# Kernel optimization log

Measured on AMD Instinct MI355X. Metric: run time of the kernel, lower is better.

The kernel has to match this reference:

```python
import jax, jax.numpy as jnp
import numpy as np

B, N, D = 8, 8192, 512
H, WIDTH = 8, 2048
DH = D // H
EPS = 1e-5


def _ln(x, g, b):
    m = jnp.mean(x, axis=-1, keepdims=True)
    v = jnp.mean(jnp.square(x - m), axis=-1, keepdims=True)
    return (x - m) * jax.lax.rsqrt(v + EPS) * g + b


def setup_inputs() -> dict:
    key = jax.random.key(0)
    ks = jax.random.split(key, 16)
    s = 0.02
    return {
        "x": jax.random.normal(ks[0], (B, N, D), dtype=jnp.float32),
        "mask": jnp.ones((B, N), dtype=jnp.float32),
        "Wq": jax.random.normal(ks[1], (D, D), dtype=jnp.float32) * s,
        "bq": jnp.zeros((D,), dtype=jnp.float32),
        "Wk": jax.random.normal(ks[2], (D, D), dtype=jnp.float32) * s,
        "bk": jnp.zeros((D,), dtype=jnp.float32),
        "Wv": jax.random.normal(ks[3], (D, D), dtype=jnp.float32) * s,
        "bv": jnp.zeros((D,), dtype=jnp.float32),
        "q_alpha": jax.random.normal(ks[4], (H, DH), dtype=jnp.float32),
        "k_beta": jax.random.normal(ks[5], (H, DH), dtype=jnp.float32),
        "Wo": jax.random.normal(ks[6], (D, D), dtype=jnp.float32) * s,
        "bo": jnp.zeros((D,), dtype=jnp.float32),
        "ln0_g": jnp.ones((D,), dtype=jnp.float32),
        "ln0_b": jnp.zeros((D,), dtype=jnp.float32),
        "ln1_g": jnp.ones((D,), dtype=jnp.float32),
        "ln1_b": jnp.zeros((D,), dtype=jnp.float32),
        "W1": jax.random.normal(ks[7], (WIDTH, D), dtype=jnp.float32) * s,
        "b1": jnp.zeros((WIDTH,), dtype=jnp.float32),
        "W2": jax.random.normal(ks[8], (D, WIDTH), dtype=jnp.float32) * s,
        "b2": jnp.zeros((D,), dtype=jnp.float32),
    }


def reference(x, mask, Wq, bq, Wk, bk, Wv, bv, q_alpha, k_beta, Wo, bo,
              ln0_g, ln0_b, ln1_g, ln1_b, W1, b1, W2, b2):
    scale = DH ** -0.5
    mask_ = mask[..., None]                       # [B,N,1]
    valid = (mask != 0)[..., None]                # [B,N,1] bool, broadcast over H

    residual = x
    xn = _ln(x, ln0_g, ln0_b) * mask_

    Q = (xn @ Wq.T + bq).reshape(B, N, H, DH)
    K = (xn @ Wk.T + bk).reshape(B, N, H, DH)
    V = (xn @ Wv.T + bv).reshape(B, N, H, DH)

    # stage 1: global query pooling
    alpha = jnp.einsum('bnhd,hd->bnh', Q, q_alpha) * scale
    alpha = jnp.where(valid, alpha, -jnp.inf)
    alpha = jax.nn.softmax(alpha, axis=1)         # softmax over N
    global_q = jnp.einsum('bnhd,bnh->bhd', Q, alpha)

    # stage 2: global value pooling
    P = K * global_q[:, None]                     # [B,N,H,DH]
    beta = jnp.einsum('bnhd,hd->bnh', P, k_beta) * scale
    beta = jnp.where(valid, beta, -jnp.inf)
    beta = jax.nn.softmax(beta, axis=1)
    global_v = jnp.einsum('bnhd,bnh->bhd', V, beta)

    out = (Q + global_v[:, None]).reshape(B, N, D)
    out = out @ Wo.T + bo
    x = residual + out

    residual = x
    xn = _ln(x, ln1_g, ln1_b)
    h = jax.nn.gelu(xn @ W1.T + b1, approximate=False)
    h = jax.nn.gelu(h @ W2.T + b2, approximate=False)
    x = residual + h
    x = x * mask_
    return x
```

## Files before the change

kernel.cpp:

```cpp
#include <hip/hip_runtime.h>
#include <hip/hip_bf16.h>
#include <hip/hip_fp8.h>
#include <math.h>

typedef short s8v __attribute__((ext_vector_type(8)));
typedef short s4v __attribute__((ext_vector_type(4)));
typedef __bf16 bf8v __attribute__((ext_vector_type(8)));
typedef float f4v __attribute__((ext_vector_type(4)));
typedef long l2v __attribute__((ext_vector_type(2)));

#define GLOBAL_AS __attribute__((address_space(1)))
#define LDS_AS __attribute__((address_space(3)))

static __device__ __forceinline__ float bf2f(ushort u) {
  return __builtin_bit_cast(float, (unsigned int)u << 16);
}
static __device__ __forceinline__ ushort f2bf(float f) {
  unsigned int u = __builtin_bit_cast(unsigned int, f);
  u += 0x7FFFu + ((u >> 16) & 1u);
  return (ushort)(u >> 16);
}
static __device__ __forceinline__ unsigned char f2fp8(float f) {
#if __has_builtin(__builtin_amdgcn_cvt_pk_fp8_f32)
  int p = __builtin_amdgcn_cvt_pk_fp8_f32(f, f, 0, false);
  return (unsigned char)(p & 0xFF);
#else
  __hip_fp8_e4m3 v(f);
  return (unsigned char)v.__x;
#endif
}
static __device__ __forceinline__ float gelu_f(float v) {
  float t = v * v;
  float u = v * (0.0356774081f * t + 0.7978845608f);
  float e = __expf(-2.0f * u);
  return v * __builtin_amdgcn_rcpf(1.0f + e);
}
static __device__ __forceinline__ float wave_max_f(float v) {
  #pragma unroll
  for (int o = 32; o >= 1; o >>= 1) v = fmaxf(v, __shfl_xor(v, o));
  return v;
}
static __device__ __forceinline__ float wave_sum_f(float v) {
  #pragma unroll
  for (int o = 32; o >= 1; o >>= 1) v += __shfl_xor(v, o);
  return v;
}
static __device__ __forceinline__ void gload16(const void* g, const void* l) {
  __builtin_amdgcn_global_load_lds(
      (const GLOBAL_AS unsigned int*)g,
      (LDS_AS unsigned int*)l, 16, 0, 0);
}

__global__ void cvt_f32_fp8il(const float* __restrict__ in,
                              unsigned char* __restrict__ out, int n, int kmask) {
  int i = (blockIdx.x * 256 + threadIdx.x) * 4;
  if (i >= n) return;
  float4 v = *(const float4*)(in + i);
  const int k = i & kmask;
  const int r = k & 63;
  const int qq = (r >> 3) & 3, h = (r >> 5) & 1, j = r & 7;
  const long o = (long)(i - r) + qq * 16 + h * 8 + j;
  uchar4 ob;
  ob.x = f2fp8(v.x * 8.f); ob.y = f2fp8(v.y * 8.f);
  ob.z = f2fp8(v.z * 8.f); ob.w = f2fp8(v.w * 8.f);
  *(uchar4*)(out + o) = ob;
}

__global__ void cvt_w1_fp8il(const float* __restrict__ in,
                             unsigned char* __restrict__ out) {
  int i = (blockIdx.x * 256 + threadIdx.x) * 4;
  const int ro = i >> 9;
  const int k4 = i & 511;
  const int g = ro >> 6, fr = ro & 63;
  const int L = fr & 15, nn = fr >> 4;
  const int sr = g * 64 + ((L >> 1) & 1) * 32 + (L >> 2) * 8 + (L & 1) * 4 + nn;
  float4 v = *(const float4*)(in + (long)sr * 512 + k4);
  const int r = k4 & 63;
  const int o = (k4 - r) + ((r >> 3) & 3) * 16 + (r >> 5) * 8 + (r & 7);
  uchar4 ob;
  ob.x = f2fp8(v.x * 8.f); ob.y = f2fp8(v.y * 8.f);
  ob.z = f2fp8(v.z * 8.f); ob.w = f2fp8(v.w * 8.f);
  *(uchar4*)(out + (long)ro * 512 + o) = ob;
}

__global__ void perm_b1(const float* __restrict__ b1, float* __restrict__ b1p) {
  const int p = blockIdx.x * 256 + threadIdx.x;
  const int g = p >> 6, r = p & 63;
  const int kc = ((r >> 3) & 1) * 32 + (r >> 4) * 8 + ((r >> 2) & 1) * 4 + (r & 3);
  b1p[p] = b1[g * 64 + kc];
}

__global__ __launch_bounds__(256) void transpose512(
    const float* __restrict__ in, float* __restrict__ out) {
  __shared__ float t[32][33];
  const int bx = blockIdx.x & 15, by = blockIdx.x >> 4;
  const int tx = threadIdx.x & 31, ty = threadIdx.x >> 5;
  #pragma unroll
  for (int i = 0; i < 4; ++i)
    t[ty + i * 8][tx] = in[(long)(by * 32 + ty + i * 8) * 512 + bx * 32 + tx];
  __syncthreads();
  #pragma unroll
  for (int i = 0; i < 4; ++i)
    out[(long)(bx * 32 + ty + i * 8) * 512 + by * 32 + tx] = t[tx][ty + i * 8];
}

__global__ __launch_bounds__(256) void wqo_kernel(
    const float* __restrict__ Wo, const float* __restrict__ Wq,
    ushort* __restrict__ WqoB)
{
  __shared__ float lO[64][33];
  __shared__ float lQ[32][65];
  const int t = threadIdx.x;
  const int bi = (blockIdx.x & 7) * 64, bj = (blockIdx.x >> 3) * 64;
  float acc[16] = {};
  for (int k0 = 0; k0 < 512; k0 += 32) {
    __syncthreads();
    {
      const int r = t >> 2, c = (t & 3) * 8;
      #pragma unroll
      for (int j = 0; j < 8; ++j) lO[r][c + j] = Wo[(long)(bi + r) * 512 + k0 + c + j];
      const int r2 = t >> 3, c2 = (t & 7) * 8;
      #pragma unroll
      for (int j = 0; j < 8; ++j) lQ[r2][c2 + j] = Wq[(long)(k0 + r2) * 512 + bj + c2 + j];
    }
    __syncthreads();
    const int j = t & 63, ig = t >> 6;
    for (int kk = 0; kk < 32; ++kk) {
      float q = lQ[kk][j];
      #pragma unroll
      for (int ii = 0; ii < 16; ++ii) acc[ii] += lO[ig * 16 + ii][kk] * q;
    }
  }
  const int j = t & 63, ig = t >> 6;
  #pragma unroll
  for (int ii = 0; ii < 16; ++ii)
    WqoB[(long)(bi + ig * 16 + ii) * 512 + bj + j] = f2bf(acc[ii]);
}

__global__ __launch_bounds__(256) void wa_kernel(
    const float* __restrict__ qa, const float* __restrict__ Wq,
    const float* __restrict__ bqv, ushort* __restrict__ waB, float* __restrict__ ca)
{
  __shared__ float ql[64];
  const int h = blockIdx.x;
  const int t = threadIdx.x;
  if (h >= 8) {
    waB[h * 512 + t] = 0; waB[h * 512 + 256 + t] = 0;
    if (t == 0) ca[h] = 0.f;
    return;
  }
  if (t < 64) ql[t] = qa[h * 64 + t];
  __syncthreads();
  #pragma unroll
  for (int half = 0; half < 2; ++half) {
    const int k = half * 256 + t;
    float s = 0;
    for (int dd = 0; dd < 64; ++dd) s += ql[dd] * Wq[(long)(h * 64 + dd) * 512 + k];
    waB[h * 512 + k] = f2bf(s);
  }
  if (t == 0) {
    float s = 0;
    for (int dd = 0; dd < 64; ++dd) s += ql[dd] * bqv[h * 64 + dd];
    ca[h] = s;
  }
}

__global__ __launch_bounds__(256) void ln_rows(
    const float* __restrict__ x, const float* __restrict__ gam,
    const float* __restrict__ bet, const float* __restrict__ mask,
    ushort* __restrict__ out)
{
  const int tid = threadIdx.x, lane = tid & 63, wv = tid >> 6;
  const long row = (long)blockIdx.x * 4 + wv;
  const float* xp = x + row * 512 + lane * 8;
  float4 a = *(const float4*)xp;
  float4 b = *(const float4*)(xp + 4);
  float s = a.x + a.y + a.z + a.w + b.x + b.y + b.z + b.w;
  float q = a.x*a.x + a.y*a.y + a.z*a.z + a.w*a.w
          + b.x*b.x + b.y*b.y + b.z*b.z + b.w*b.w;
  s = wave_sum_f(s); q = wave_sum_f(q);
  float m = s * (1.f / 512.f);
  float var = q * (1.f / 512.f) - m * m;
  float r = rsqrtf(var + 1e-5f);
  float mk = mask ? mask[row] : 1.f;
  const float* gp = gam + lane * 8;
  const float* bp = bet + lane * 8;
  float4 g0 = *(const float4*)gp, g1 = *(const float4*)(gp + 4);
  float4 c0 = *(const float4*)bp, c1 = *(const float4*)(bp + 4);
  s8v o;
  o[0] = (short)f2bf(((a.x - m) * r * g0.x + c0.x) * mk);
  o[1] = (short)f2bf(((a.y - m) * r * g0.y + c0.y) * mk);
  o[2] = (short)f2bf(((a.z - m) * r * g0.z + c0.z) * mk);
  o[3] = (short)f2bf(((a.w - m) * r * g0.w + c0.w) * mk);
  o[4] = (short)f2bf(((b.x - m) * r * g1.x + c1.x) * mk);
  o[5] = (short)f2bf(((b.y - m) * r * g1.y + c1.y) * mk);
  o[6] = (short)f2bf(((b.z - m) * r * g1.z + c1.z) * mk);
  o[7] = (short)f2bf(((b.w - m) * r * g1.w + c1.w) * mk);
  *(s8v*)(out + row * 512 + lane * 8) = o;
}

__global__ __launch_bounds__(256) void ln_rows_fp8il(
    const ushort* __restrict__ x, const float* __restrict__ gam,
    const float* __restrict__ bet, unsigned char* __restrict__ out)
{
  const int tid = threadIdx.x, lane = tid & 63, wv = tid >> 6;
  const long row = (long)blockIdx.x * 4 + wv;
  s8v v = *(const s8v*)(x + row * 512 + lane * 8);
  float xv[8];
  #pragma unroll
  for (int j = 0; j < 8; ++j) xv[j] = bf2f((ushort)v[j]);
  float s = 0.f, q = 0.f;
  #pragma unroll
  for (int j = 0; j < 8; ++j) { s += xv[j]; q += xv[j] * xv[j]; }
  s = wave_sum_f(s); q = wave_sum_f(q);
  float m = s * (1.f / 512.f);
  float var = q * (1.f / 512.f) - m * m;
  float r = rsqrtf(var + 1e-5f);
  const float* gp = gam + lane * 8;
  const float* bp = bet + lane * 8;
  float4 g0 = *(const float4*)gp, g1 = *(const float4*)(gp + 4);
  float4 c0 = *(const float4*)bp, c1 = *(const float4*)(bp + 4);
  float gg[8] = {g0.x, g0.y, g0.z, g0.w, g1.x, g1.y, g1.z, g1.w};
  float cc[8] = {c0.x, c0.y, c0.z, c0.w, c1.x, c1.y, c1.z, c1.w};
  unsigned long long pk = 0;
  #pragma unroll
  for (int j = 0; j < 8; ++j) {
    unsigned char b8 = f2fp8((xv[j] - m) * r * gg[j] + cc[j]);
    pk |= (unsigned long long)b8 << (8 * j);
  }
  *(unsigned long long*)(out + row * 512 + (lane >> 3) * 64
                         + (lane & 3) * 16 + ((lane >> 2) & 1) * 8) = pk;
}

template<int BS, int CS>
__global__ __launch_bounds__(256) void logits_k(
    const ushort* __restrict__ XN, const ushort* __restrict__ Wl,
    const float* __restrict__ cvec, const float* __restrict__ mask,
    float* __restrict__ outL)
{
  __shared__ ushort lw[16 * 512];
  const int tid = threadIdx.x, lane = tid & 63, wv = tid >> 6;
  const long r0 = (long)blockIdx.x * 64;
  const int b = (int)(r0 >> 13);
  #pragma unroll
  for (int i = 0; i < 4; ++i) {
    const int u = tid + i * 256;
    const int h2 = u >> 6, uu = u & 63;
    s8v v = *(const s8v*)(Wl + (long)b * BS + h2 * 512 + uu * 8);
    *(s8v*)(lw + h2 * 512 + (uu ^ (h2 & 7)) * 8) = v;
  }
  __syncthreads();
  const int h = lane & 15, q = lane >> 4;
  const long rw = r0 + wv * 16;
  const ushort* ap = XN + (rw + (lane & 15)) * 512 + q * 8;
  f4v acc = {};
  #pragma unroll
  for (int t = 0; t < 16; ++t) {
    bf8v a = *(const bf8v*)(ap + t * 32);
    bf8v bb = *(const bf8v*)(lw + h * 512 + (((t * 4 + q) ^ (h & 7))) * 8);
    acc = __builtin_amdgcn_mfma_f32_16x16x32_bf16(a, bb, acc, 0, 0, 0);
  }
  const float cv = cvec[b * CS + h];
  #pragma unroll
  for (int j = 0; j < 4; ++j) {
    const long n = rw + q * 4 + j;
    float v = (acc[j] + cv) * 0.125f;
    if (mask[n] == 0.f) v = -1e30f;
    if (h < 8) outL[((long)((b << 3) + h) << 13) + (n & 8191)] = v;
  }
}

__global__ __launch_bounds__(1024) void softmax_rows(float* __restrict__ L)
{
  __shared__ float red[16];
  __shared__ float bc;
  const int tid = threadIdx.x, lane = tid & 63, wv = tid >> 6;
  float* p = L + ((long)blockIdx.x << 13) + tid * 8;
  float4 v0 = *(float4*)p;
  float4 v1 = *(float4*)(p + 4);
  float m = fmaxf(fmaxf(fmaxf(v0.x, v0.y), fmaxf(v0.z, v0.w)),
                  fmaxf(fmaxf(v1.x, v1.y), fmaxf(v1.z, v1.w)));
  m = wave_max_f(m);
  if (lane == 0) red[wv] = m;
  __syncthreads();
  if (tid < 64) {
    float t = (lane < 16) ? red[lane] : -INFINITY;
    t = wave_max_f(t);
    if (lane == 0) bc = t;
  }
  __syncthreads();
  const float gm = bc;
  v0.x = __expf(v0.x - gm); v0.y = __expf(v0.y - gm);
  v0.z = __expf(v0.z - gm); v0.w = __expf(v0.w - gm);
  v1.x = __expf(v1.x - gm); v1.y = __expf(v1.y - gm);
  v1.z = __expf(v1.z - gm); v1.w = __expf(v1.w - gm);
  float s = v0.x + v0.y + v0.z + v0.w + v1.x + v1.y + v1.z + v1.w;
  s = wave_sum_f(s);
  __syncthreads();
  if (lane == 0) red[wv] = s;
  __syncthreads();
  if (tid < 64) {
    float t = (lane < 16) ? red[lane] : 0.f;
    t = wave_sum_f(t);
    if (lane == 0) bc = t;
  }
  __syncthreads();
  const float inv = 1.0f / bc;
  v0.x *= inv; v0.y *= inv; v0.z *= inv; v0.w *= inv;
  v1.x *= inv; v1.y *= inv; v1.z *= inv; v1.w *= inv;
  *(float4*)p = v0;
  *(float4*)(p + 4) = v1;
}

__global__ __launch_bounds__(256) void pool_w(
    const ushort* __restrict__ XN, const float* __restrict__ wbuf,
    float* __restrict__ part)
{
  __shared__ float wlds[128][8];
  __shared__ float cmb[4][512];
  const int tid = threadIdx.x;
  const int b = blockIdx.x >> 6, ch = blockIdx.x & 63;
  const long g0 = ((long)b << 13) + ch * 128;
  if (tid < 128) {
    #pragma unroll
    for (int h = 0; h < 8; ++h)
      wlds[tid][h] = wbuf[(((long)(b * 8 + h)) << 13) + ch * 128 + tid];
  }
  __syncthreads();
  const int rg = tid >> 6, c8 = (tid & 63) * 8;
  f4v acc[8][2] = {};
  for (int it = 0; it < 32; ++it) {
    const int r = it * 4 + rg;
    s8v xv = *(const s8v*)(XN + (g0 + r) * 512 + c8);
    float xf[8];
    #pragma unroll
    for (int j = 0; j < 8; ++j) xf[j] = bf2f((ushort)xv[j]);
    #pragma unroll
    for (int h = 0; h < 8; ++h) {
      const float w = wlds[r][h];
      #pragma unroll
      for (int j = 0; j < 8; ++j) acc[h][j >> 2][j & 3] += w * xf[j];
    }
  }
  #pragma unroll
  for (int h = 0; h < 8; ++h) {
    __syncthreads();
    #pragma unroll
    for (int j = 0; j < 8; ++j) cmb[rg][c8 + j] = acc[h][j >> 2][j & 3];
    __syncthreads();
    const int col = tid * 2;
    float s0 = cmb[0][col] + cmb[1][col] + cmb[2][col] + cmb[3][col];
    float s1 = cmb[0][col + 1] + cmb[1][col + 1] + cmb[2][col + 1] + cmb[3][col + 1];
    *(float2*)(part + (((long)blockIdx.x * 8 + h) << 9) + col) = make_float2(s0, s1);
  }
}

__global__ __launch_bounds__(256) void combine_px(
    const float* __restrict__ part, float* __restrict__ px)
{
  const int bh = blockIdx.x;
  const int b = bh >> 3, h = bh & 7;
  const int col = threadIdx.x * 2;
  float s0 = 0.f, s1 = 0.f;
  for (int ch = 0; ch < 64; ++ch) {
    const float* p = part + (((long)((b * 64 + ch) * 8 + h)) << 9) + col;
    s0 += p[0]; s1 += p[1];
  }
  px[(bh << 9) + col] = s0;
  px[(bh << 9) + col + 1] = s1;
}

__global__ __launch_bounds__(64) void prep_gq_wb(
    const float* __restrict__ px, const float* __restrict__ WqT,
    const float* __restrict__ bqv, const float* __restrict__ kbv,
    const float* __restrict__ Wk, const float* __restrict__ bkv,
    ushort* __restrict__ wbB, float* __restrict__ cbs)
{
  __shared__ float pxl[512];
  __shared__ float gkb[64];
  const int bh = blockIdx.x, b = bh >> 3, h = bh & 7, d = threadIdx.x;
  #pragma unroll
  for (int i = 0; i < 8; ++i) pxl[d + i * 64] = px[(bh << 9) + d + i * 64];
  __syncthreads();
  float acc = bqv[h * 64 + d];
  for (int c = 0; c < 512; ++c) acc += pxl[c] * WqT[(long)c * 512 + h * 64 + d];
  gkb[d] = acc * kbv[h * 64 + d];
  __syncthreads();
  float s[8] = {};
  for (int dd = 0; dd < 64; ++dd) {
    const float g = gkb[dd];
    const float* wr = Wk + (long)(h * 64 + dd) * 512 + d;
    #pragma unroll
    for (int ki = 0; ki < 8; ++ki) s[ki] += g * wr[ki * 64];
  }
  #pragma unroll
  for (int ki = 0; ki < 8; ++ki)
    wbB[(long)(b * 16 + h) * 512 + d + ki * 64] = f2bf(s[ki]);
  if (d == 0) {
    float t = 0.f;
    for (int dd = 0; dd < 64; ++dd) t += gkb[dd] * bkv[h * 64 + dd];
    cbs[b * 16 + h] = t;
  }
  if (h == 0) {
    #pragma unroll
    for (int hp = 8; hp < 16; ++hp)
      for (int k = d; k < 512; k += 64) wbB[(long)(b * 16 + hp) * 512 + k] = 0;
    if (d < 8) cbs[b * 16 + 8 + d] = 0.f;
  }
}

__global__ __launch_bounds__(64) void prep_gv(
    const float* __restrict__ pv, const float* __restrict__ WvT,
    const float* __restrict__ bvv, const float* __restrict__ bqv,
    float* __restrict__ gvb)
{
  __shared__ float pxl[512];
  const int bh = blockIdx.x, b = bh >> 3, h = bh & 7, d = threadIdx.x;
  #pragma unroll
  for (int i = 0; i < 8; ++i) pxl[d + i * 64] = pv[(bh << 9) + d + i * 64];
  __syncthreads();
  float acc = bvv[h * 64 + d] + bqv[h * 64 + d];
  for (int c = 0; c < 512; ++c) acc += pxl[c] * WvT[(long)c * 512 + h * 64 + d];
  gvb[b * 512 + h * 64 + d] = acc;
}

__global__ __launch_bounds__(256) void bias_gv(
    const float* __restrict__ gv, const float* __restrict__ Wo,
    const float* __restrict__ bo, float* __restrict__ bo2) {
  const int b = blockIdx.x;
  const int n = blockIdx.y * 256 + threadIdx.x;
  const float* g = gv + b * 512;
  const float* w = Wo + (long)n * 512;
  float acc = 0.f;
  for (int d = 0; d < 512; d += 4) {
    float4 wv4 = *(const float4*)(w + d);
    acc += g[d] * wv4.x + g[d + 1] * wv4.y + g[d + 2] * wv4.z + g[d + 3] * wv4.w;
  }
  bo2[b * 512 + n] = bo[n] + acc;
}

#define MFMA_(d,a,b) d = __builtin_amdgcn_mfma_f32_16x16x32_bf16(a, b, d, 0, 0, 0)

template<int EPI, int LDA, int NN, int KK>
__global__ __launch_bounds__(512, 4) void gemmP(
    const ushort* __restrict__ A, const ushort* __restrict__ W,
    const float* __restrict__ bias, const void* __restrict__ resid,
    const float* __restrict__ mask, void* __restrict__ Out)
{
  constexpr int NBX = NN / 256;
  constexpr int NT = KK / 32;
  __shared__ __align__(16) ushort lds[3][12288];
  const int tid = threadIdx.x;
  const int lane = tid & 63;
  const int w = tid >> 6;
  const int wm = w >> 2, wn = w & 3;

  const int nwg = gridDim.x;
  const int cpx = nwg >> 3;
  const int wg = (blockIdx.x & 7) * cpx + (blockIdx.x >> 3);
  const int bx = wg % NBX, by = wg / NBX;
  const long bm = (long)by * 128;
  const int bn = bx * 256;

  const int scr = tid >> 2, sls = tid & 3;
  const int akU = ((sls ^ (scr & 3) ^ ((scr >> 2) & 3))) * 8;
  const ushort* asrc = A + (bm + scr) * (long)LDA + akU;
  const int rbe = (scr & 31) + ((scr >> 5) << 6);
  const ushort* besrc = W + (long)(bn + rbe) * KK + akU;
  const ushort* bosrc = W + (long)(bn + rbe + 32) * KK + akU;

#define STG(b_, Tt) { \
    gload16(asrc + (Tt) * 32, &lds[b_][tid * 8]); \
    gload16(besrc + (Tt) * 32, &lds[b_][4096 + tid * 8]); \
    gload16(bosrc + (Tt) * 32, &lds[b_][8192 + tid * 8]); }

  STG(0, 0);
  STG(1, 1);

  f4v acc[4][4] = {};

  const int L = lane & 15, q = lane >> 4;
  const int soff = (q ^ (lane & 3) ^ ((lane >> 2) & 3)) * 8;
  const int abase = (wm * 64 + L) * 32 + soff;
  const int bbase = 4096 + (wn * 32 + L) * 32 + soff;

  asm volatile("s_waitcnt vmcnt(3)" ::: "memory");
  asm volatile("s_barrier" ::: "memory");

  for (int T = 0; T < NT; ++T) {
    const ushort* Lp = &lds[T % 3][0];
    bf8v aR[4], bR[4];
    #pragma unroll
    for (int m = 0; m < 4; ++m) aR[m] = *(const bf8v*)(Lp + abase + m * 512);
    bR[0] = *(const bf8v*)(Lp + bbase);
    bR[1] = *(const bf8v*)(Lp + bbase + 512);
    bR[2] = *(const bf8v*)(Lp + bbase + 4096);
    bR[3] = *(const bf8v*)(Lp + bbase + 4096 + 512);
    if (T + 2 < NT) {
      STG((T + 2) % 3, T + 2);
      asm volatile("s_waitcnt vmcnt(3)" ::: "memory");
    } else {
      asm volatile("s_waitcnt vmcnt(0)" ::: "memory");
    }
    asm volatile("s_barrier" ::: "memory");
    __builtin_amdgcn_s_setprio(1);
    #pragma unroll
    for (int m = 0; m < 4; ++m)
      #pragma unroll
      for (int n = 0; n < 4; ++n)
        MFMA_(acc[m][n], aR[m], bR[n]);
    __builtin_amdgcn_s_setprio(0);
  }
#undef STG

  const int colb = bn + wn * 64 + L;
  const long rowb = bm + wm * 64 + q * 4;
  const float* biasp = bias + ((bm >> 13) << 9);
  #pragma unroll
  for (int m = 0; m < 4; ++m) {
    #pragma unroll
    for (int j = 0; j < 4; ++j) {
      const long row = rowb + m * 16 + j;
      #pragma unroll
      for (int n = 0; n < 4; ++n) {
        const int col = colb + n * 16;
        float v = acc[m][n][j] + biasp[col];
        const long idx = row * (long)NN + col;
        ((ushort*)Out)[idx] = f2bf(v + ((const float*)resid)[idx]);
      }
    }
  }
}

template<int EPI, int NN, int KK>
__global__ __launch_bounds__(512, 4) void gemmF8(
    const unsigned char* __restrict__ A, const unsigned char* __restrict__ W,
    const float* __restrict__ bias, const void* __restrict__ resid,
    const float* __restrict__ mask, void* __restrict__ Out)
{
  constexpr int NBX = NN / 256;
  constexpr int NT = KK / 64;
  __shared__ __align__(16) unsigned char lds8[3][24576];
  const int tid = threadIdx.x;
  const int lane = tid & 63;
  const int w = tid >> 6;
  const int wm = w >> 2, wn = w & 3;

  const int nwg = gridDim.x;
  const int cpx = nwg >> 3;
  const int wg = (blockIdx.x & 7) * cpx + (blockIdx.x >> 3);
  const int bx = wg % NBX, by = wg / NBX;
  const long bm = (long)by * 128;
  const int bn = bx * 256;

  const int srow = tid >> 2;
  const int sgu = (tid & 3) ^ ((srow >> 1) & 3);
  const unsigned char* asrc = A + (bm + srow) * (long)KK + sgu * 16;
  const unsigned char* b0src = W + (long)(bn + srow) * KK + sgu * 16;
  const unsigned char* b1src = W + (long)(bn + 128 + srow) * KK + sgu * 16;

#define STG8(bf_, Tt) { \
    gload16(asrc + (Tt) * 64, &lds8[bf_][tid * 16]); \
    gload16(b0src + (Tt) * 64, &lds8[bf_][8192 + tid * 16]); \
    gload16(b1src + (Tt) * 64, &lds8[bf_][16384 + tid * 16]); }

  STG8(0, 0);
  STG8(1, 1);

  f4v acc[4][4] = {};

  const int L = lane & 15, q = lane >> 4;
  const int ua = (q ^ ((L >> 1) & 3)) * 16;
  const int arow = (wm * 64 + L) * 64;
  const int brow = 8192 + (wn * 64 + L) * 64;

  asm volatile("s_waitcnt vmcnt(3)" ::: "memory");
  asm volatile("s_barrier" ::: "memory");

  for (int T = 0; T < NT; ++T) {
    const unsigned char* Lp = &lds8[T % 3][0];
    l2v aV[4], bV[4];
    #pragma unroll
    for (int m = 0; m < 4; ++m) aV[m] = *(const l2v*)(Lp + arow + m * 1024 + ua);
    #pragma unroll
    for (int n = 0; n < 4; ++n) bV[n] = *(const l2v*)(Lp + brow + n * 1024 + ua);
    if (T + 2 < NT) {
      STG8((T + 2) % 3, T + 2);
      asm volatile("s_waitcnt vmcnt(3)" ::: "memory");
    } else {
      asm volatile("s_waitcnt vmcnt(0)" ::: "memory");
    }
    asm volatile("s_barrier" ::: "memory");
    __builtin_amdgcn_s_setprio(1);
    #pragma unroll
    for (int m = 0; m < 4; ++m)
      #pragma unroll
      for (int n = 0; n < 4; ++n) {
        acc[m][n] = __builtin_amdgcn_mfma_f32_16x16x32_fp8_fp8(
            aV[m][0], bV[n][0], acc[m][n], 0, 0, 0);
        acc[m][n] = __builtin_amdgcn_mfma_f32_16x16x32_fp8_fp8(
            aV[m][1], bV[n][1], acc[m][n], 0, 0, 0);
      }
    __builtin_amdgcn_s_setprio(0);
  }
#undef STG8

  const long rowb = bm + wm * 64 + q * 4;
  const int gbase = bn + wn * 64;
  if constexpr (EPI == 7) {
    const float4 bp4 = *(const float4*)(bias + gbase + 4 * L);
    #pragma unroll
    for (int m = 0; m < 4; ++m) {
      #pragma unroll
      for (int j = 0; j < 4; ++j) {
        const long row = rowb + m * 16 + j;
        float e0 = gelu_f(acc[m][0][j] * 0.125f + bp4.x);
        float e1 = gelu_f(acc[m][1][j] * 0.125f + bp4.y);
        float e2 = gelu_f(acc[m][2][j] * 0.125f + bp4.z);
        float e3 = gelu_f(acc[m][3][j] * 0.125f + bp4.w);
        unsigned int pw;
#if __has_builtin(__builtin_amdgcn_cvt_pk_fp8_f32)
        int t0 = __builtin_amdgcn_cvt_pk_fp8_f32(e0, e1, 0, false);
        pw = (unsigned int)__builtin_amdgcn_cvt_pk_fp8_f32(e2, e3, t0, true);
#else
        pw = (unsigned int)f2fp8(e0) | ((unsigned int)f2fp8(e1) << 8)
           | ((unsigned int)f2fp8(e2) << 16) | ((unsigned int)f2fp8(e3) << 24);
#endif
        *(unsigned int*)((unsigned char*)Out + row * (long)NN + gbase + 4 * L) = pw;
      }
    }
  } else {
    #pragma unroll
    for (int m = 0; m < 4; ++m) {
      #pragma unroll
      for (int j = 0; j < 4; ++j) {
        const long row = rowb + m * 16 + j;
        const float mk = mask[row];
        #pragma unroll
        for (int n = 0; n < 4; ++n) {
          const int col = gbase + n * 16 + L;
          float v = acc[m][n][j] * 0.125f + bias[col];
          const long idx = row * (long)NN + col;
          ((float*)Out)[idx] =
              (bf2f(((const ushort*)resid)[idx]) + gelu_f(v)) * mk;
        }
      }
    }
  }
}

extern "C" void kernel_launch(void* const* d_in, const int* in_sizes, int n_in,
                              void* d_out, int out_size, void* d_ws, size_t ws_size,
                              hipStream_t stream) {
  const float* x    = (const float*)d_in[0];
  const float* mask = (const float*)d_in[1];
  const float* Wq   = (const float*)d_in[2];
  const float* bq   = (const float*)d_in[3];
  const float* Wk   = (const float*)d_in[4];
  const float* bk   = (const float*)d_in[5];
  const float* Wv   = (const float*)d_in[6];
  const float* bv   = (const float*)d_in[7];
  const float* qa   = (const float*)d_in[8];
  const float* kb   = (const float*)d_in[9];
  const float* Wo   = (const float*)d_in[10];
  const float* bo   = (const float*)d_in[11];
  const float* g0   = (const float*)d_in[12];
  const float* be0  = (const float*)d_in[13];
  const float* g1   = (const float*)d_in[14];
  const float* be1  = (const float*)d_in[15];
  const float* W1   = (const float*)d_in[16];
  const float* b1   = (const float*)d_in[17];
  const float* W2   = (const float*)d_in[18];
  const float* b2   = (const float*)d_in[19];
  float* out = (float*)d_out;

  const int M = 65536;
  char* ws = (char*)d_ws;
  const size_t MB = 1024 * 1024;
  ushort* XN  = (ushort*)(ws);
  ushort* X1  = (ushort*)(ws + 64 * MB);
  unsigned char* XN1F = (unsigned char*)(ws + 128 * MB);
  unsigned char* H1F  = (unsigned char*)(ws + 192 * MB);
  float*  AL  = (float*)(ws + 320 * MB);
  float*  BL  = (float*)(ws + 322 * MB);
  float*  PART= (float*)(ws + 324 * MB);
  char* base = ws + 448 * MB;
  unsigned char* W1F = (unsigned char*)(base);
  unsigned char* W2F = (unsigned char*)(base + 2 * MB);
  ushort* WqoB = (ushort*)(base + 4 * MB);
  float*  WqT  = (float*)(base + 4 * MB + 512 * 1024);
  float*  WvT  = (float*)(base + 5 * MB + 512 * 1024);
  ushort* waB  = (ushort*)(base + 6 * MB + 512 * 1024);
  ushort* wbB  = (ushort*)(base + 6 * MB + 528 * 1024);
  float*  ca   = (float*)(base + 6 * MB + 656 * 1024);
  float*  cbs  = (float*)(base + 6 * MB + 660 * 1024);
  float*  PX   = (float*)(base + 6 * MB + 664 * 1024);
  float*  PV   = (float*)(base + 6 * MB + 792 * 1024);
  float*  GVB  = (float*)(base + 6 * MB + 920 * 1024);
  float*  BO2  = (float*)(base + 6 * MB + 936 * 1024);
  float*  B1P  = (float*)(base + 6 * MB + 952 * 1024);

  cvt_w1_fp8il<<<1024, 256, 0, stream>>>(W1, W1F);
  perm_b1<<<8, 256, 0, stream>>>(b1, B1P);
  cvt_f32_fp8il<<<1024, 256, 0, stream>>>(W2, W2F, 1048576, 2047);
  wqo_kernel<<<64, 256, 0, stream>>>(Wo, Wq, WqoB);
  wa_kernel<<<16, 256, 0, stream>>>(qa, Wq, bq, waB, ca);
  transpose512<<<256, 256, 0, stream>>>(Wq, WqT);
  transpose512<<<256, 256, 0, stream>>>(Wv, WvT);

  ln_rows<<<M / 4, 256, 0, stream>>>(x, g0, be0, mask, XN);

  logits_k<0, 0><<<1024, 256, 0, stream>>>(XN, waB, ca, mask, AL);
  softmax_rows<<<64, 1024, 0, stream>>>(AL);
  pool_w<<<512, 256, 0, stream>>>(XN, AL, PART);
  combine_px<<<64, 256, 0, stream>>>(PART, PX);
  prep_gq_wb<<<64, 64, 0, stream>>>(PX, WqT, bq, kb, Wk, bk, wbB, cbs);

  logits_k<8192, 16><<<1024, 256, 0, stream>>>(XN, wbB, cbs, mask, BL);
  softmax_rows<<<64, 1024, 0, stream>>>(BL);
  pool_w<<<512, 256, 0, stream>>>(XN, BL, PART);
  combine_px<<<64, 256, 0, stream>>>(PART, PV);
  prep_gv<<<64, 64, 0, stream>>>(PV, WvT, bv, bq, GVB);
  bias_gv<<<dim3(8, 2), 256, 0, stream>>>(GVB, Wo, bo, BO2);

  gemmP<5, 512, 512, 512><<<2 * (M / 128), 512, 0, stream>>>(
      XN, WqoB, BO2, x, nullptr, X1);

  ln_rows_fp8il<<<M / 4, 256, 0, stream>>>(X1, g1, be1, XN1F);

  gemmF8<7, 2048, 512><<<8 * (M / 128), 512, 0, stream>>>(
      XN1F, W1F, B1P, nullptr, nullptr, H1F);
  gemmF8<8, 512, 2048><<<2 * (M / 128), 512, 0, stream>>>(
      H1F, W2F, b2, X1, mask, out);
}
```

Measured before the change: 590.4 us.

## Fuse LN0 with alpha logits, stage logits tile in LDS, merge combine+prep kernels

LayerNorm0 now also computes the eight alpha logits per row with wave reductions against the LDS-cached pooled weight. This removes one logits_k launch and its re-read of XN. The remaining logits_k copies its 64x512 bf16 XN tile into swizzled LDS with async loads before the MFMA loop. The partial-sum combine kernels are folded into the prep kernels, dropping two launches and the PX/PV round trips. The costs are more LDS per logits block (lower occupancy) and serial per-head wave reductions in the LN kernel.

Result: no change. 585.6 us (-0.8%).

```diff
diff --git a/kernel.cpp b/kernel.cpp
--- a/kernel.cpp
+++ b/kernel.cpp
@@ -165,38 +165,66 @@
   }
 }
 
-__global__ __launch_bounds__(256) void ln_rows(
+__global__ __launch_bounds__(256) void ln0_alpha(
     const float* __restrict__ x, const float* __restrict__ gam,
     const float* __restrict__ bet, const float* __restrict__ mask,
-    ushort* __restrict__ out)
-{
+    const ushort* __restrict__ waB, const float* __restrict__ ca,
+    ushort* __restrict__ out, float* __restrict__ AL)
+{
+  __shared__ ushort wal[8 * 512];
   const int tid = threadIdx.x, lane = tid & 63, wv = tid >> 6;
-  const long row = (long)blockIdx.x * 4 + wv;
-  const float* xp = x + row * 512 + lane * 8;
-  float4 a = *(const float4*)xp;
-  float4 b = *(const float4*)(xp + 4);
-  float s = a.x + a.y + a.z + a.w + b.x + b.y + b.z + b.w;
-  float q = a.x*a.x + a.y*a.y + a.z*a.z + a.w*a.w
-          + b.x*b.x + b.y*b.y + b.z*b.z + b.w*b.w;
-  s = wave_sum_f(s); q = wave_sum_f(q);
-  float m = s * (1.f / 512.f);
-  float var = q * (1.f / 512.f) - m * m;
-  float r = rsqrtf(var + 1e-5f);
-  float mk = mask ? mask[row] : 1.f;
+  *(s8v*)(wal + tid * 8) = *(const s8v*)(waB + tid * 8);
+  *(s8v*)(wal + 2048 + tid * 8) = *(const s8v*)(waB + 2048 + tid * 8);
   const float* gp = gam + lane * 8;
   const float* bp = bet + lane * 8;
   float4 g0 = *(const float4*)gp, g1 = *(const float4*)(gp + 4);
   float4 c0 = *(const float4*)bp, c1 = *(const float4*)(bp + 4);
-  s8v o;
-  o[0] = (short)f2bf(((a.x - m) * r * g0.x + c0.x) * mk);
-  o[1] = (short)f2bf(((a.y - m) * r * g0.y + c0.y) * mk);
-  o[2] = (short)f2bf(((a.z - m) * r * g0.z + c0.z) * mk);
-  o[3] = (short)f2bf(((a.w - m) * r * g0.w + c0.w) * mk);
-  o[4] = (short)f2bf(((b.x - m) * r * g1.x + c1.x) * mk);
-  o[5] = (short)f2bf(((b.y - m) * r * g1.y + c1.y) * mk);
-  o[6] = (short)f2bf(((b.z - m) * r * g1.z + c1.z) * mk);
-  o[7] = (short)f2bf(((b.w - m) * r * g1.w + c1.w) * mk);
-  *(s8v*)(out + row * 512 + lane * 8) = o;
+  const float gg[8] = {g0.x, g0.y, g0.z, g0.w, g1.x, g1.y, g1.z, g1.w};
+  const float cc[8] = {c0.x, c0.y, c0.z, c0.w, c1.x, c1.y, c1.z, c1.w};
+  __syncthreads();
+  const long row0 = (long)blockIdx.x * 16 + wv * 4;
+  for (int rr = 0; rr < 4; ++rr) {
+    const long row = row0 + rr;
+    const float* xp = x + row * 512 + lane * 8;
+    float4 a = *(const float4*)xp;
+    float4 b = *(const float4*)(xp + 4);
+    float s = a.x + a.y + a.z + a.w + b.x + b.y + b.z + b.w;
+    float q = a.x*a.x + a.y*a.y + a.z*a.z + a.w*a.w
+            + b.x*b.x + b.y*b.y + b.z*b.z + b.w*b.w;
+    s = wave_sum_f(s); q = wave_sum_f(q);
+    const float m = s * (1.f / 512.f);
+    const float var = q * (1.f / 512.f) - m * m;
+    const float r = rsqrtf(var + 1e-5f);
+    const float mk = mask[row];
+    const float xin[8] = {a.x, a.y, a.z, a.w, b.x, b.y, b.z, b.w};
+    float of[8];
+    s8v o;
+    #pragma unroll
+    for (int j = 0; j < 8; ++j) {
+      of[j] = ((xin[j] - m) * r * gg[j] + cc[j]) * mk;
+      o[j] = (short)f2bf(of[j]);
+    }
+    *(s8v*)(out + row * 512 + lane * 8) = o;
+    float dh[8];
+    #pragma unroll
+    for (int h = 0; h < 8; ++h) {
+      s8v wa8 = *(const s8v*)(wal + h * 512 + lane * 8);
+      float d = 0.f;
+      #pragma unroll
+      for (int j = 0; j < 8; ++j) d += of[j] * bf2f((ushort)wa8[j]);
+      dh[h] = wave_sum_f(d);
+    }
+    if (lane == 0) {
+      const int bb = (int)(row >> 13);
+      const int n = (int)(row & 8191);
+      #pragma unroll
+      for (int h = 0; h < 8; ++h) {
+        float lg = (dh[h] + ca[h]) * 0.125f;
+        if (mk == 0.f) lg = -1e30f;
+        AL[((long)((bb << 3) + h) << 13) + n] = lg;
+      }
+    }
+  }
 }
 
 __global__ __launch_bounds__(256) void ln_rows_fp8il(
@@ -239,9 +267,17 @@
     float* __restrict__ outL)
 {
   __shared__ ushort lw[16 * 512];
+  __shared__ __align__(16) ushort lx[64 * 512];
   const int tid = threadIdx.x, lane = tid & 63, wv = tid >> 6;
   const long r0 = (long)blockIdx.x * 64;
   const int b = (int)(r0 >> 13);
+  #pragma unroll
+  for (int i = 0; i < 16; ++i) {
+    const int U = i * 256 + tid;
+    const int r = U >> 6, u1 = U & 63;
+    const int us = u1 ^ (r & 7);
+    gload16(XN + (r0 + r) * 512 + us * 8, lx + (long)U * 8);
+  }
   #pragma unroll
   for (int i = 0; i < 4; ++i) {
     const int u = tid + i * 256;
@@ -251,16 +287,17 @@
   }
   __syncthreads();
   const int h = lane & 15, q = lane >> 4;
-  const long rw = r0 + wv * 16;
-  const ushort* ap = XN + (rw + (lane & 15)) * 512 + q * 8;
+  const int rloc = wv * 16 + (lane & 15);
+  const ushort* axp = lx + rloc * 512;
   f4v acc = {};
   #pragma unroll
   for (int t = 0; t < 16; ++t) {
-    bf8v a = *(const bf8v*)(ap + t * 32);
+    bf8v a = *(const bf8v*)(axp + (((t * 4 + q) ^ (rloc & 7))) * 8);
     bf8v bb = *(const bf8v*)(lw + h * 512 + (((t * 4 + q) ^ (h & 7))) * 8);
     acc = __builtin_amdgcn_mfma_f32_16x16x32_bf16(a, bb, acc, 0, 0, 0);
   }
   const float cv = cvec[b * CS + h];
+  const long rw = r0 + wv * 16;
   #pragma unroll
   for (int j = 0; j < 4; ++j) {
     const long n = rw + q * 4 + j;
@@ -355,73 +392,83 @@
   }
 }
 
-__global__ __launch_bounds__(256) void combine_px(
-    const float* __restrict__ part, float* __restrict__ px)
-{
-  const int bh = blockIdx.x;
-  const int b = bh >> 3, h = bh & 7;
-  const int col = threadIdx.x * 2;
-  float s0 = 0.f, s1 = 0.f;
-  for (int ch = 0; ch < 64; ++ch) {
-    const float* p = part + (((long)((b * 64 + ch) * 8 + h)) << 9) + col;
-    s0 += p[0]; s1 += p[1];
-  }
-  px[(bh << 9) + col] = s0;
-  px[(bh << 9) + col + 1] = s1;
-}
-
-__global__ __launch_bounds__(64) void prep_gq_wb(
-    const float* __restrict__ px, const float* __restrict__ WqT,
+__global__ __launch_bounds__(256) void combine_prep1(
+    const float* __restrict__ part, const float* __restrict__ WqT,
     const float* __restrict__ bqv, const float* __restrict__ kbv,
     const float* __restrict__ Wk, const float* __restrict__ bkv,
     ushort* __restrict__ wbB, float* __restrict__ cbs)
 {
   __shared__ float pxl[512];
   __shared__ float gkb[64];
-  const int bh = blockIdx.x, b = bh >> 3, h = bh & 7, d = threadIdx.x;
-  #pragma unroll
-  for (int i = 0; i < 8; ++i) pxl[d + i * 64] = px[(bh << 9) + d + i * 64];
-  __syncthreads();
-  float acc = bqv[h * 64 + d];
-  for (int c = 0; c < 512; ++c) acc += pxl[c] * WqT[(long)c * 512 + h * 64 + d];
-  gkb[d] = acc * kbv[h * 64 + d];
-  __syncthreads();
-  float s[8] = {};
-  for (int dd = 0; dd < 64; ++dd) {
-    const float g = gkb[dd];
-    const float* wr = Wk + (long)(h * 64 + dd) * 512 + d;
-    #pragma unroll
-    for (int ki = 0; ki < 8; ++ki) s[ki] += g * wr[ki * 64];
-  }
-  #pragma unroll
-  for (int ki = 0; ki < 8; ++ki)
-    wbB[(long)(b * 16 + h) * 512 + d + ki * 64] = f2bf(s[ki]);
-  if (d == 0) {
-    float t = 0.f;
-    for (int dd = 0; dd < 64; ++dd) t += gkb[dd] * bkv[h * 64 + dd];
-    cbs[b * 16 + h] = t;
-  }
-  if (h == 0) {
-    #pragma unroll
-    for (int hp = 8; hp < 16; ++hp)
-      for (int k = d; k < 512; k += 64) wbB[(long)(b * 16 + hp) * 512 + k] = 0;
-    if (d < 8) cbs[b * 16 + 8 + d] = 0.f;
-  }
-}
-
-__global__ __launch_bounds__(64) void prep_gv(
-    const float* __restrict__ pv, const float* __restrict__ WvT,
+  const int bh = blockIdx.x, b = bh >> 3, h = bh & 7;
+  const int tid = threadIdx.x;
+  {
+    const int col = tid * 2;
+    float s0 = 0.f, s1 = 0.f;
+    for (int ch = 0; ch < 64; ++ch) {
+      const float* p = part + (((long)((b * 64 + ch) * 8 + h)) << 9) + col;
+      s0 += p[0]; s1 += p[1];
+    }
+    pxl[col] = s0; pxl[col + 1] = s1;
+  }
+  __syncthreads();
+  if (tid < 64) {
+    const int d = tid;
+    float acc = bqv[h * 64 + d];
+    for (int c = 0; c < 512; ++c) acc += pxl[c] * WqT[(long)c * 512 + h * 64 + d];
+    gkb[d] = acc * kbv[h * 64 + d];
+  }
+  __syncthreads();
+  if (tid < 64) {
+    const int d = tid;
+    float s[8] = {};
+    for (int dd = 0; dd < 64; ++dd) {
+      const float g = gkb[dd];
+      const float* wr = Wk + (long)(h * 64 + dd) * 512 + d;
+      #pragma unroll
+      for (int ki = 0; ki < 8; ++ki) s[ki] += g * wr[ki * 64];
+    }
+    #pragma unroll
+    for (int ki = 0; ki < 8; ++ki)
+      wbB[(long)(b * 16 + h) * 512 + d + ki * 64] = f2bf(s[ki]);
+    if (d == 0) {
+      float t = 0.f;
+      for (int dd = 0; dd < 64; ++dd) t += gkb[dd] * bkv[h * 64 + dd];
+      cbs[b * 16 + h] = t;
+    }
+    if (h == 0) {
+      #pragma unroll
+      for (int hp = 8; hp < 16; ++hp)
+        for (int k = d; k < 512; k += 64) wbB[(long)(b * 16 + hp) * 512 + k] = 0;
+      if (d < 8) cbs[b * 16 + 8 + d] = 0.f;
+    }
+  }
+}
+
+__global__ __launch_bounds__(256) void combine_prep2(
+    const float* __restrict__ part, const float* __restrict__ WvT,
     const float* __restrict__ bvv, const float* __restrict__ bqv,
     float* __restrict__ gvb)
 {
   __shared__ float pxl[512];
-  const int bh = blockIdx.x, b = bh >> 3, h = bh & 7, d = threadIdx.x;
-  #pragma unroll
-  for (int i = 0; i < 8; ++i) pxl[d + i * 64] = pv[(bh << 9) + d + i * 64];
-  __syncthreads();
-  float acc = bvv[h * 64 + d] + bqv[h * 64 + d];
-  for (int c = 0; c < 512; ++c) acc += pxl[c] * WvT[(long)c * 512 + h * 64 + d];
-  gvb[b * 512 + h * 64 + d] = acc;
+  const int bh = blockIdx.x, b = bh >> 3, h = bh & 7;
+  const int tid = threadIdx.x;
+  {
+    const int col = tid * 2;
+    float s0 = 0.f, s1 = 0.f;
+    for (int ch = 0; ch < 64; ++ch) {
+      const float* p = part + (((long)((b * 64 + ch) * 8 + h)) << 9) + col;
+      s0 += p[0]; s1 += p[1];
+    }
+    pxl[col] = s0; pxl[col + 1] = s1;
+  }
+  __syncthreads();
+  if (tid < 64) {
+    const int d = tid;
+    float acc = bvv[h * 64 + d] + bqv[h * 64 + d];
+    for (int c = 0; c < 512; ++c) acc += pxl[c] * WvT[(long)c * 512 + h * 64 + d];
+    gvb[b * 512 + h * 64 + d] = acc;
+  }
 }
 
 __global__ __launch_bounds__(256) void bias_gv(
@@ -694,8 +741,6 @@
   ushort* wbB  = (ushort*)(base + 6 * MB + 528 * 1024);
   float*  ca   = (float*)(base + 6 * MB + 656 * 1024);
   float*  cbs  = (float*)(base + 6 * MB + 660 * 1024);
-  float*  PX   = (float*)(base + 6 * MB + 664 * 1024);
-  float*  PV   = (float*)(base + 6 * MB + 792 * 1024);
   float*  GVB  = (float*)(base + 6 * MB + 920 * 1024);
   float*  BO2  = (float*)(base + 6 * MB + 936 * 1024);
   float*  B1P  = (float*)(base + 6 * MB + 952 * 1024);
@@ -708,19 +753,16 @@
   transpose512<<<256, 256, 0, stream>>>(Wq, WqT);
   transpose512<<<256, 256, 0, stream>>>(Wv, WvT);
 
-  ln_rows<<<M / 4, 256, 0, stream>>>(x, g0, be0, mask, XN);
-
-  logits_k<0, 0><<<1024, 256, 0, stream>>>(XN, waB, ca, mask, AL);
+  ln0_alpha<<<M / 16, 256, 0, stream>>>(x, g0, be0, mask, waB, ca, XN, AL);
+
   softmax_rows<<<64, 1024, 0, stream>>>(AL);
   pool_w<<<512, 256, 0, stream>>>(XN, AL, PART);
-  combine_px<<<64, 256, 0, stream>>>(PART, PX);
-  prep_gq_wb<<<64, 64, 0, stream>>>(PX, WqT, bq, kb, Wk, bk, wbB, cbs);
+  combine_prep1<<<64, 256, 0, stream>>>(PART, WqT, bq, kb, Wk, bk, wbB, cbs);
 
   logits_k<8192, 16><<<1024, 256, 0, stream>>>(XN, wbB, cbs, mask, BL);
   softmax_rows<<<64, 1024, 0, stream>>>(BL);
   pool_w<<<512, 256, 0, stream>>>(XN, BL, PART);
-  combine_px<<<64, 256, 0, stream>>>(PART, PV);
-  prep_gv<<<64, 64, 0, stream>>>(PV, WvT, bv, bq, GVB);
+  combine_prep2<<<64, 256, 0, stream>>>(PART, WvT, bv, bq, GVB);
   bias_gv<<<dim3(8, 2), 256, 0, stream>>>(GVB, Wo, bo, BO2);
 
   gemmP<5, 512, 512, 512><<<2 * (M / 128), 512, 0, stream>>>(
```
